# Optimization experiments

Measured on AMD Instinct MI355X. Metric: run time of the kernel, lower is better.

Reference implementation:

```python
import jax, jax.numpy as jnp
import numpy as np

GAMMA = 0.015625  # 1/D


def setup_inputs() -> dict:
    key = jax.random.key(0)
    k1, k2 = jax.random.split(key)
    data = jax.random.normal(k1, (8192, 64), dtype=jnp.float32)
    support_vectors = jax.random.normal(k2, (8192, 64), dtype=jnp.float32)
    return {"data": data, "support_vectors": support_vectors}


def reference(data, support_vectors):
    # RBF kernel matrix: K[i,j] = exp(-gamma * ||data_i - sv_j||^2)
    # instead of the original per-row Python loop.
    x_sq = jnp.sum(data * data, axis=1, keepdims=True)          # [N, 1]
    y_sq = jnp.sum(support_vectors * support_vectors, axis=1)   # [M]
    cross = data @ support_vectors.T                             # [N, M]
    d2 = jnp.maximum(x_sq + y_sq[None, :] - 2.0 * cross, 0.0)
    return jnp.exp(-GAMMA * d2)
```

## Files before the change

kernel.cpp:

```cpp
#include <hip/hip_runtime.h>
#include <hip/hip_bf16.h>
#include <string.h>

#define GAMMA 0.015625f
#define D 64

typedef short bf16x8 __attribute__((ext_vector_type(8)));
typedef float floatx4 __attribute__((ext_vector_type(4)));

__device__ __forceinline__ bf16x8 cvt8(const float* __restrict__ p, float& ss) {
    const float4 a = *(const float4*)p;
    const float4 b = *(const float4*)(p + 4);
    const float f[8] = {a.x, a.y, a.z, a.w, b.x, b.y, b.z, b.w};
    bf16x8 r;
#pragma unroll
    for (int i = 0; i < 8; ++i) {
        __hip_bfloat16 h = __float2bfloat16(f[i]);
        short s;
        memcpy(&s, &h, sizeof(short));
        r[i] = s;
        const float bv = __bfloat162float(h);
        ss = fmaf(bv, bv, ss);
    }
    return r;
}

__global__ __launch_bounds__(256) void rbf_fused(const float* __restrict__ A,
                                                 const float* __restrict__ B,
                                                 float* __restrict__ out,
                                                 int M) {
    const int wid  = threadIdx.x >> 6;
    const int lane = threadIdx.x & 63;
    const int quad = lane >> 4;
    const int l16  = lane & 15;

    const long row0 = (long)blockIdx.y * 128 + (wid >> 1) * 64;
    const long col0 = (long)blockIdx.x * 128 + (wid & 1) * 64;

    bf16x8 af[4][2], bfr[4][2];
    float xnorm[4];
    float ynorm[4];

#pragma unroll
    for (int mb = 0; mb < 4; ++mb) {
        const float* p = A + (row0 + mb * 16 + l16) * D + quad * 8;
        float s = 0.f;
        af[mb][0] = cvt8(p, s);
        af[mb][1] = cvt8(p + 32, s);
        s += __shfl_xor(s, 16, 64);
        s += __shfl_xor(s, 32, 64);
        xnorm[mb] = s;
    }
#pragma unroll
    for (int nb = 0; nb < 4; ++nb) {
        const float* p = B + (col0 + nb * 16 + l16) * D + quad * 8;
        float s = 0.f;
        bfr[nb][0] = cvt8(p, s);
        bfr[nb][1] = cvt8(p + 32, s);
        s += __shfl_xor(s, 16, 64);
        s += __shfl_xor(s, 32, 64);
        ynorm[nb] = s;
    }

    floatx4 acc[4][4];
#pragma unroll
    for (int mb = 0; mb < 4; ++mb)
#pragma unroll
        for (int nb = 0; nb < 4; ++nb)
            acc[mb][nb] = (floatx4){0.f, 0.f, 0.f, 0.f};

#pragma unroll
    for (int k = 0; k < 2; ++k)
#pragma unroll
        for (int mb = 0; mb < 4; ++mb)
#pragma unroll
            for (int nb = 0; nb < 4; ++nb)
                acc[mb][nb] = __builtin_amdgcn_mfma_f32_16x16x32_bf16(
                    af[mb][k], bfr[nb][k], acc[mb][nb], 0, 0, 0);

#pragma unroll
    for (int mb = 0; mb < 4; ++mb) {
        float xn[4];
#pragma unroll
        for (int r = 0; r < 4; ++r)
            xn[r] = __shfl(xnorm[mb], quad * 4 + r, 64);
#pragma unroll
        for (int nb = 0; nb < 4; ++nb) {
            const long col = col0 + nb * 16 + l16;
            const float yn = ynorm[nb];
#pragma unroll
            for (int r = 0; r < 4; ++r) {
                const long row = row0 + mb * 16 + quad * 4 + r;
                float d2 = fmaxf(xn[r] + yn - 2.0f * acc[mb][nb][r], 0.0f);
                out[row * (long)M + col] = __expf(-GAMMA * d2);
            }
        }
    }
}

__global__ __launch_bounds__(256) void rbf_naive(const float* __restrict__ X,
                                                 const float* __restrict__ Y,
                                                 float* __restrict__ out,
                                                 int N, int M) {
    long idx = (long)blockIdx.x * blockDim.x + threadIdx.x;
    if (idx >= (long)N * M) return;
    long i = idx / M, j = idx % M;
    float s = 0.0f;
#pragma unroll
    for (int k = 0; k < D; ++k) {
        float d = X[i * D + k] - Y[j * D + k];
        s = fmaf(d, d, s);
    }
    out[idx] = __expf(-GAMMA * s);
}

extern "C" void kernel_launch(void* const* d_in, const int* in_sizes, int n_in,
                              void* d_out, int out_size, void* d_ws, size_t ws_size,
                              hipStream_t stream) {
    const float* data = (const float*)d_in[0];
    const float* sv   = (const float*)d_in[1];
    float* out = (float*)d_out;
    const int N = in_sizes[0] / D;
    const int M = in_sizes[1] / D;

    if ((N % 128) == 0 && (M % 128) == 0) {
        dim3 grid(M / 128, N / 128);
        hipLaunchKernelGGL(rbf_fused, grid, dim3(256), 0, stream,
                           data, sv, out, M);
    } else {
        long total = (long)N * M;
        long blocks = (total + 255) / 256;
        hipLaunchKernelGGL(rbf_naive, dim3((unsigned)blocks), dim3(256), 0, stream,
                           data, sv, out, N, M);
    }
}
```

Measured before the change: 303.6 us.

## Switch to 32x32 MFMA tiles and loop each block over four column tiles

Replaces the 16x16x32 bf16 MFMA with the 32x32x16 variant and changes the fragment layout to match. Each block now loops over four 128-column tiles, reusing its converted A fragments and row norms across them. This cuts the grid size and repeated A loads and conversions, but serialises more work per block. The output is 256 MB of fp32 writes, so the kernel is likely store-bound, and the store pattern per lane changes to 32-wide rows.

```diff
diff --git a/kernel.cpp b/kernel.cpp
--- a/kernel.cpp
+++ b/kernel.cpp
@@ -4,9 +4,10 @@
 
 #define GAMMA 0.015625f
 #define D 64
+#define CT 4
 
 typedef short bf16x8 __attribute__((ext_vector_type(8)));
-typedef float floatx4 __attribute__((ext_vector_type(4)));
+typedef float floatx16 __attribute__((ext_vector_type(16)));
 
 __device__ __forceinline__ bf16x8 cvt8(const float* __restrict__ p, float& ss) {
     const float4 a = *(const float4*)p;
@@ -25,74 +26,74 @@
     return r;
 }
 
-__global__ __launch_bounds__(256) void rbf_fused(const float* __restrict__ A,
-                                                 const float* __restrict__ B,
-                                                 float* __restrict__ out,
-                                                 int M) {
+__global__ __launch_bounds__(256) void rbf_fused32(const float* __restrict__ A,
+                                                   const float* __restrict__ B,
+                                                   float* __restrict__ out,
+                                                   int M) {
     const int wid  = threadIdx.x >> 6;
     const int lane = threadIdx.x & 63;
-    const int quad = lane >> 4;
-    const int l16  = lane & 15;
+    const int r32  = lane & 31;
+    const int h    = lane >> 5;
 
     const long row0 = (long)blockIdx.y * 128 + (wid >> 1) * 64;
-    const long col0 = (long)blockIdx.x * 128 + (wid & 1) * 64;
+    const long colW = (long)blockIdx.x * (128 * CT) + (wid & 1) * 64;
 
-    bf16x8 af[4][2], bfr[4][2];
-    float xnorm[4];
-    float ynorm[4];
-
+    bf16x8 af[2][4];
+    float xnorm[2];
 #pragma unroll
-    for (int mb = 0; mb < 4; ++mb) {
-        const float* p = A + (row0 + mb * 16 + l16) * D + quad * 8;
+    for (int mb = 0; mb < 2; ++mb) {
+        const float* p = A + (row0 + mb * 32 + r32) * D + h * 8;
         float s = 0.f;
-        af[mb][0] = cvt8(p, s);
-        af[mb][1] = cvt8(p + 32, s);
-        s += __shfl_xor(s, 16, 64);
+#pragma unroll
+        for (int ks = 0; ks < 4; ++ks)
+            af[mb][ks] = cvt8(p + ks * 16, s);
         s += __shfl_xor(s, 32, 64);
         xnorm[mb] = s;
     }
+
+    for (int ct = 0; ct < CT; ++ct) {
+        const long colT = colW + (long)ct * 128;
+
+        bf16x8 bfr[2][4];
+        float ynorm[2];
 #pragma unroll
-    for (int nb = 0; nb < 4; ++nb) {
-        const float* p = B + (col0 + nb * 16 + l16) * D + quad * 8;
-        float s = 0.f;
-        bfr[nb][0] = cvt8(p, s);
-        bfr[nb][1] = cvt8(p + 32, s);
-        s += __shfl_xor(s, 16, 64);
-        s += __shfl_xor(s, 32, 64);
-        ynorm[nb] = s;
-    }
+        for (int nb = 0; nb < 2; ++nb) {
+            const float* p = B + (colT + nb * 32 + r32) * D + h * 8;
+            float s = 0.f;
+#pragma unroll
+            for (int ks = 0; ks < 4; ++ks)
+                bfr[nb][ks] = cvt8(p + ks * 16, s);
+            s += __shfl_xor(s, 32, 64);
+            ynorm[nb] = s;
+        }
 
-    floatx4 acc[4][4];
+        floatx16 acc[2][2] = {};
 #pragma unroll
-    for (int mb = 0; mb < 4; ++mb)
+        for (int ks = 0; ks < 4; ++ks)
 #pragma unroll
-        for (int nb = 0; nb < 4; ++nb)
-            acc[mb][nb] = (floatx4){0.f, 0.f, 0.f, 0.f};
+            for (int mb = 0; mb < 2; ++mb)
+#pragma unroll
+                for (int nb = 0; nb < 2; ++nb)
+                    acc[mb][nb] = __builtin_amdgcn_mfma_f32_32x32x16_bf16(
+                        af[mb][ks], bfr[nb][ks], acc[mb][nb], 0, 0, 0);
 
 #pragma unroll
-    for (int k = 0; k < 2; ++k)
+        for (int mb = 0; mb < 2; ++mb) {
+            float xnv[16];
 #pragma unroll
-        for (int mb = 0; mb < 4; ++mb)
+            for (int rg = 0; rg < 16; ++rg)
+                xnv[rg] = __shfl(xnorm[mb], (rg & 3) + 8 * (rg >> 2) + 4 * h, 64);
 #pragma unroll
-            for (int nb = 0; nb < 4; ++nb)
-                acc[mb][nb] = __builtin_amdgcn_mfma_f32_16x16x32_bf16(
-                    af[mb][k], bfr[nb][k], acc[mb][nb], 0, 0, 0);
-
+            for (int nb = 0; nb < 2; ++nb) {
+                const long col = colT + nb * 32 + r32;
+                const float yn = ynorm[nb];
+                float* op = out + (row0 + mb * 32) * (long)M + col;
 #pragma unroll
-    for (int mb = 0; mb < 4; ++mb) {
-        float xn[4];
-#pragma unroll
-        for (int r = 0; r < 4; ++r)
-            xn[r] = __shfl(xnorm[mb], quad * 4 + r, 64);
-#pragma unroll
-        for (int nb = 0; nb < 4; ++nb) {
-            const long col = col0 + nb * 16 + l16;
-            const float yn = ynorm[nb];
-#pragma unroll
-            for (int r = 0; r < 4; ++r) {
-                const long row = row0 + mb * 16 + quad * 4 + r;
-                float d2 = fmaxf(xn[r] + yn - 2.0f * acc[mb][nb][r], 0.0f);
-                out[row * (long)M + col] = __expf(-GAMMA * d2);
+                for (int rg = 0; rg < 16; ++rg) {
+                    const int rl = (rg & 3) + 8 * (rg >> 2) + 4 * h;
+                    float d2 = fmaxf(xnv[rg] + yn - 2.0f * acc[mb][nb][rg], 0.0f);
+                    op[(long)rl * M] = __expf(-GAMMA * d2);
+                }
             }
         }
     }
@@ -123,9 +124,9 @@
     const int N = in_sizes[0] / D;
     const int M = in_sizes[1] / D;
 
-    if ((N % 128) == 0 && (M % 128) == 0) {
-        dim3 grid(M / 128, N / 128);
-        hipLaunchKernelGGL(rbf_fused, grid, dim3(256), 0, stream,
+    if ((N % 128) == 0 && (M % (128 * CT)) == 0) {
+        dim3 grid(M / (128 * CT), N / 128);
+        hipLaunchKernelGGL(rbf_fused32, grid, dim3(256), 0, stream,
                            data, sv, out, M);
     } else {
         long total = (long)N * M;
```

Result: no change. 300.3 us (-1.1%).
